# Performance work log

Hardware: AMD Instinct MI355X
Metric: run time of the kernel (lower is better)

The kernel has to match this reference:

```python
import jax, jax.numpy as jnp
import numpy as np

NUM_USERS = 1_000_000
NUM_ITEMS = 100_000
NUM_GROUPS = 500_000
EMB = 32           # forced by reshape (1, 4*32)
GROUP_SIZE = 3     # forced: 3 members + 1 item = 4 rows
B = 131_072


def setup_inputs() -> dict:
    key = jax.random.key(0)
    ks = jax.random.split(key, 12)
    return {
        "group_inputs": jax.random.randint(ks[0], (B,), 0, NUM_GROUPS),
        "item_inputs": jax.random.randint(ks[1], (B,), 0, NUM_ITEMS),
        "members": jax.random.randint(ks[2], (NUM_GROUPS, GROUP_SIZE), 0, NUM_USERS),
        "user_emb": jax.random.normal(ks[3], (NUM_USERS, EMB), jnp.float32) * 0.05,
        "item_emb": jax.random.normal(ks[4], (NUM_ITEMS, EMB - 18), jnp.float32) * 0.05,
        "genres": jax.random.uniform(ks[5], (NUM_ITEMS, 18), jnp.float32),
        "attn_W": jax.random.normal(ks[6], (4 * EMB, 3), jnp.float32) * 0.05,
        "attn_b": jax.random.normal(ks[7], (3,), jnp.float32) * 0.05,
        "pred_W1": jax.random.normal(ks[8], (3 * EMB, 8), jnp.float32) * 0.05,
        "pred_b1": jax.random.normal(ks[9], (8,), jnp.float32) * 0.05,
        "pred_W2": jax.random.normal(ks[10], (8, 1), jnp.float32) * 0.05,
        "pred_b2": jax.random.normal(ks[11], (1,), jnp.float32) * 0.05,
    }


def reference(group_inputs, item_inputs, members, user_emb, item_emb, genres,
              attn_W, attn_b, pred_W1, pred_b1, pred_W2, pred_b2):
    # item embedding: 14-d latent concat 18-d genre features -> [B, 32]
    it_e = jnp.concatenate([item_emb[item_inputs], genres[item_inputs]], axis=1)
    # members of each group -> [B, 3, 32]
    mem_e = user_emb[members[group_inputs]]
    # concat 3 member rows + 1 item row, flatten to [B, 128]
    gi = jnp.concatenate([mem_e, it_e[:, None, :]], axis=1).reshape(-1, 4 * EMB)
    # NOTE: source ConcatAttentionLayer returns the raw linear output (softmax
    # is computed but discarded), so attention "weights" are raw logits. [B, 3]
    at_wt = gi @ attn_W + attn_b
    # weighted sum of member embeddings -> [B, 32]
    g = jnp.einsum("bk,bkd->bd", at_wt, mem_e)
    new = jnp.concatenate([g * it_e, g, it_e], axis=1)  # [B, 96]
    h = jax.nn.relu(new @ pred_W1 + pred_b1)
    y = jax.nn.sigmoid(h @ pred_W2 + pred_b2)  # [B, 1]
    return y
```

## Files before the change

### kernel.cpp

```cpp
#include <hip/hip_runtime.h>
#include <math.h>

#define EMB 32

__global__ __launch_bounds__(256, 4) void bahdanau_fused(
    const int* __restrict__ group_inputs,
    const int* __restrict__ item_inputs,
    const int* __restrict__ members,
    const float* __restrict__ user_emb,
    const float* __restrict__ item_emb,
    const float* __restrict__ genres,
    const float* __restrict__ attn_W,
    const float* __restrict__ attn_b,
    const float* __restrict__ pred_W1,
    const float* __restrict__ pred_b1,
    const float* __restrict__ pred_W2,
    const float* __restrict__ pred_b2,
    float* __restrict__ out)
{
    __shared__ float s_aWT[3 * 128];
    __shared__ float s_W1T[8 * 96];
    __shared__ float s_ab[3];
    __shared__ float s_b1[8];
    __shared__ float s_W2[8];
    __shared__ float s_b2[1];

    const int tid = threadIdx.x;
    const int t = tid & 3;
    const int grp = tid >> 2;
    const int ebase = blockIdx.x * 128 + grp * 2;
    const int dbase = t * 8;

    const int g0 = group_inputs[ebase], g1 = group_inputs[ebase + 1];
    const int i0 = item_inputs[ebase],  i1 = item_inputs[ebase + 1];

    int m0[3], m1[3];
#pragma unroll
    for (int j = 0; j < 3; ++j) {
        m0[j] = members[3 * g0 + j];
        m1[j] = members[3 * g1 + j];
    }

    float itv0[8], itv1[8];
#pragma unroll
    for (int i = 0; i < 4; ++i) {
        const int d = dbase + 2 * i;
        const float2* p0 = (d < 14)
            ? (const float2*)(item_emb + (size_t)i0 * 14 + d)
            : (const float2*)(genres   + (size_t)i0 * 18 + (d - 14));
        const float2* p1 = (d < 14)
            ? (const float2*)(item_emb + (size_t)i1 * 14 + d)
            : (const float2*)(genres   + (size_t)i1 * 18 + (d - 14));
        const float2 a = *p0, b = *p1;
        itv0[2 * i]     = a.x; itv0[2 * i + 1] = a.y;
        itv1[2 * i]     = b.x; itv1[2 * i + 1] = b.y;
    }

    float mem0[3][8], mem1[3][8];
#pragma unroll
    for (int j = 0; j < 3; ++j) {
        const float4* p0 = (const float4*)(user_emb + (size_t)m0[j] * EMB + dbase);
        const float4* p1 = (const float4*)(user_emb + (size_t)m1[j] * EMB + dbase);
        float4 a = p0[0], b = p0[1], c = p1[0], d = p1[1];
        mem0[j][0] = a.x; mem0[j][1] = a.y; mem0[j][2] = a.z; mem0[j][3] = a.w;
        mem0[j][4] = b.x; mem0[j][5] = b.y; mem0[j][6] = b.z; mem0[j][7] = b.w;
        mem1[j][0] = c.x; mem1[j][1] = c.y; mem1[j][2] = c.z; mem1[j][3] = c.w;
        mem1[j][4] = d.x; mem1[j][5] = d.y; mem1[j][6] = d.z; mem1[j][7] = d.w;
    }

    for (int i = tid; i < 3 * 128; i += 256) {
        int k = i >> 7, d = i & 127;
        s_aWT[i] = attn_W[d * 3 + k];
    }
    for (int i = tid; i < 8 * 96; i += 256) {
        int c = i / 96, r = i - c * 96;
        s_W1T[i] = pred_W1[r * 8 + c];
    }
    if (tid < 3) s_ab[tid] = attn_b[tid];
    else if (tid < 11) s_b1[tid - 3] = pred_b1[tid - 3];
    else if (tid < 19) s_W2[tid - 11] = pred_W2[tid - 11];
    else if (tid == 19) s_b2[0] = pred_b2[0];
    __syncthreads();

    float aw0[3], aw1[3];
#pragma unroll
    for (int k = 0; k < 3; ++k) {
        float a0 = 0.f, a1 = 0.f;
#pragma unroll
        for (int j = 0; j < 3; ++j) {
            const float4* wp = (const float4*)&s_aWT[k * 128 + j * 32 + dbase];
            float4 wl = wp[0], wh = wp[1];
            float w[8] = {wl.x, wl.y, wl.z, wl.w, wh.x, wh.y, wh.z, wh.w};
#pragma unroll
            for (int i = 0; i < 8; ++i) {
                a0 = fmaf(mem0[j][i], w[i], a0);
                a1 = fmaf(mem1[j][i], w[i], a1);
            }
        }
        {
            const float4* wp = (const float4*)&s_aWT[k * 128 + 96 + dbase];
            float4 wl = wp[0], wh = wp[1];
            float w[8] = {wl.x, wl.y, wl.z, wl.w, wh.x, wh.y, wh.z, wh.w};
#pragma unroll
            for (int i = 0; i < 8; ++i) {
                a0 = fmaf(itv0[i], w[i], a0);
                a1 = fmaf(itv1[i], w[i], a1);
            }
        }
        aw0[k] = a0; aw1[k] = a1;
    }
#pragma unroll
    for (int k = 0; k < 3; ++k) {
        float v0 = aw0[k];
        v0 += __shfl_xor(v0, 1, 4);
        v0 += __shfl_xor(v0, 2, 4);
        aw0[k] = v0 + s_ab[k];
        float v1 = aw1[k];
        v1 += __shfl_xor(v1, 1, 4);
        v1 += __shfl_xor(v1, 2, 4);
        aw1[k] = v1 + s_ab[k];
    }

    float gv0[8], gv1[8], git0[8], git1[8];
#pragma unroll
    for (int i = 0; i < 8; ++i) {
        gv0[i] = aw0[0] * mem0[0][i] + aw0[1] * mem0[1][i] + aw0[2] * mem0[2][i];
        gv1[i] = aw1[0] * mem1[0][i] + aw1[1] * mem1[1][i] + aw1[2] * mem1[2][i];
        git0[i] = gv0[i] * itv0[i];
        git1[i] = gv1[i] * itv1[i];
    }

    float ph0[8], ph1[8];
#pragma unroll
    for (int c = 0; c < 8; ++c) {
        float a0 = 0.f, a1 = 0.f;
        const float4* wp0 = (const float4*)&s_W1T[c * 96 + dbase];
        const float4* wp1 = (const float4*)&s_W1T[c * 96 + 32 + dbase];
        const float4* wp2 = (const float4*)&s_W1T[c * 96 + 64 + dbase];
        float4 al = wp0[0], ah = wp0[1];
        float4 bl = wp1[0], bh = wp1[1];
        float4 cl = wp2[0], ch = wp2[1];
        float wa[8] = {al.x, al.y, al.z, al.w, ah.x, ah.y, ah.z, ah.w};
        float wb[8] = {bl.x, bl.y, bl.z, bl.w, bh.x, bh.y, bh.z, bh.w};
        float wc[8] = {cl.x, cl.y, cl.z, cl.w, ch.x, ch.y, ch.z, ch.w};
#pragma unroll
        for (int i = 0; i < 8; ++i) {
            a0 = fmaf(git0[i], wa[i], a0);
            a0 = fmaf(gv0[i],  wb[i], a0);
            a0 = fmaf(itv0[i], wc[i], a0);
            a1 = fmaf(git1[i], wa[i], a1);
            a1 = fmaf(gv1[i],  wb[i], a1);
            a1 = fmaf(itv1[i], wc[i], a1);
        }
        ph0[c] = a0; ph1[c] = a1;
    }

    float hq[8];
#pragma unroll
    for (int c = 0; c < 8; ++c) {
        float v0 = ph0[c];
        v0 += __shfl_xor(v0, 1, 4);
        v0 += __shfl_xor(v0, 2, 4);
        float v1 = ph1[c];
        v1 += __shfl_xor(v1, 1, 4);
        v1 += __shfl_xor(v1, 2, 4);
        hq[c] = (t == 0) ? v0 : v1;
    }

    if (t < 2) {
        float y = s_b2[0];
#pragma unroll
        for (int c = 0; c < 8; ++c) {
            float h = fmaxf(hq[c] + s_b1[c], 0.0f);
            y = fmaf(h, s_W2[c], y);
        }
        y = 1.0f / (1.0f + expf(-y));
        out[ebase + t] = y;
    }
}

extern "C" void kernel_launch(void* const* d_in, const int* in_sizes, int n_in,
                              void* d_out, int out_size, void* d_ws, size_t ws_size,
                              hipStream_t stream) {
    const int*   group_inputs = (const int*)d_in[0];
    const int*   item_inputs  = (const int*)d_in[1];
    const int*   members      = (const int*)d_in[2];
    const float* user_emb     = (const float*)d_in[3];
    const float* item_emb     = (const float*)d_in[4];
    const float* genres       = (const float*)d_in[5];
    const float* attn_W       = (const float*)d_in[6];
    const float* attn_b       = (const float*)d_in[7];
    const float* pred_W1      = (const float*)d_in[8];
    const float* pred_b1      = (const float*)d_in[9];
    const float* pred_W2      = (const float*)d_in[10];
    const float* pred_b2      = (const float*)d_in[11];
    float* out = (float*)d_out;

    const int B = in_sizes[0];
    const int blocks = B / 128;

    bahdanau_fused<<<blocks, 256, 0, stream>>>(
        group_inputs, item_inputs, members, user_emb, item_emb, genres,
        attn_W, attn_b, pred_W1, pred_b1, pred_W2, pred_b2, out);
}
```

Measured before the change: 208.6 us.

## Give each wavefront a private weight copy to drop block barrier and split element pipelines

```diff
diff --git a/kernel.cpp b/kernel.cpp
--- a/kernel.cpp
+++ b/kernel.cpp
@@ -18,22 +18,40 @@
     const float* __restrict__ pred_b2,
     float* __restrict__ out)
 {
-    __shared__ float s_aWT[3 * 128];
-    __shared__ float s_W1T[8 * 96];
-    __shared__ float s_ab[3];
-    __shared__ float s_b1[8];
-    __shared__ float s_W2[8];
-    __shared__ float s_b2[1];
-
-    const int tid = threadIdx.x;
+    __shared__ float smem[4 * 1184];
+
+    const int tid  = threadIdx.x;
+    const int lane = tid & 63;
+    float* sw = smem + (tid >> 6) * 1184;
+
     const int t = tid & 3;
     const int grp = tid >> 2;
     const int ebase = blockIdx.x * 128 + grp * 2;
     const int dbase = t * 8;
 
-    const int g0 = group_inputs[ebase], g1 = group_inputs[ebase + 1];
-    const int i0 = item_inputs[ebase],  i1 = item_inputs[ebase + 1];
-
+    const int2 gpair = *(const int2*)&group_inputs[ebase];
+    const int2 ipair = *(const int2*)&item_inputs[ebase];
+
+#pragma unroll
+    for (int it = 0; it < 19; ++it) {
+        const int i = lane + it * 64;
+        float v;
+        if (i < 384) {
+            const int k = i >> 7, d = i & 127;
+            v = attn_W[d * 3 + k];
+        } else if (i < 1152) {
+            const int r2 = i - 384, c = r2 / 96, r = r2 - c * 96;
+            v = pred_W1[r * 8 + c];
+        } else if (i < 1155) v = attn_b[i - 1152];
+        else if (i < 1163)   v = pred_b1[i - 1155];
+        else if (i < 1171)   v = pred_W2[i - 1163];
+        else                 v = pred_b2[0];
+        if (i < 1172) sw[i] = v;
+        else if (i < 1184) sw[i] = 0.0f;
+    }
+
+    const int g0 = gpair.x, g1 = gpair.y;
+    const int i0 = ipair.x, i1 = ipair.y;
     int m0[3], m1[3];
 #pragma unroll
     for (int j = 0; j < 3; ++j) {
@@ -48,132 +66,154 @@
         const float2* p0 = (d < 14)
             ? (const float2*)(item_emb + (size_t)i0 * 14 + d)
             : (const float2*)(genres   + (size_t)i0 * 18 + (d - 14));
+        const float2 a = *p0;
+        itv0[2 * i] = a.x; itv0[2 * i + 1] = a.y;
+    }
+#pragma unroll
+    for (int i = 0; i < 4; ++i) {
+        const int d = dbase + 2 * i;
         const float2* p1 = (d < 14)
             ? (const float2*)(item_emb + (size_t)i1 * 14 + d)
             : (const float2*)(genres   + (size_t)i1 * 18 + (d - 14));
-        const float2 a = *p0, b = *p1;
-        itv0[2 * i]     = a.x; itv0[2 * i + 1] = a.y;
-        itv1[2 * i]     = b.x; itv1[2 * i + 1] = b.y;
+        const float2 b = *p1;
+        itv1[2 * i] = b.x; itv1[2 * i + 1] = b.y;
     }
 
     float mem0[3][8], mem1[3][8];
 #pragma unroll
     for (int j = 0; j < 3; ++j) {
         const float4* p0 = (const float4*)(user_emb + (size_t)m0[j] * EMB + dbase);
-        const float4* p1 = (const float4*)(user_emb + (size_t)m1[j] * EMB + dbase);
-        float4 a = p0[0], b = p0[1], c = p1[0], d = p1[1];
+        float4 a = p0[0], b = p0[1];
         mem0[j][0] = a.x; mem0[j][1] = a.y; mem0[j][2] = a.z; mem0[j][3] = a.w;
         mem0[j][4] = b.x; mem0[j][5] = b.y; mem0[j][6] = b.z; mem0[j][7] = b.w;
+    }
+#pragma unroll
+    for (int j = 0; j < 3; ++j) {
+        const float4* p1 = (const float4*)(user_emb + (size_t)m1[j] * EMB + dbase);
+        float4 c = p1[0], d = p1[1];
         mem1[j][0] = c.x; mem1[j][1] = c.y; mem1[j][2] = c.z; mem1[j][3] = c.w;
         mem1[j][4] = d.x; mem1[j][5] = d.y; mem1[j][6] = d.z; mem1[j][7] = d.w;
     }
 
-    for (int i = tid; i < 3 * 128; i += 256) {
-        int k = i >> 7, d = i & 127;
-        s_aWT[i] = attn_W[d * 3 + k];
-    }
-    for (int i = tid; i < 8 * 96; i += 256) {
-        int c = i / 96, r = i - c * 96;
-        s_W1T[i] = pred_W1[r * 8 + c];
-    }
-    if (tid < 3) s_ab[tid] = attn_b[tid];
-    else if (tid < 11) s_b1[tid - 3] = pred_b1[tid - 3];
-    else if (tid < 19) s_W2[tid - 11] = pred_W2[tid - 11];
-    else if (tid == 19) s_b2[0] = pred_b2[0];
-    __syncthreads();
-
-    float aw0[3], aw1[3];
-#pragma unroll
-    for (int k = 0; k < 3; ++k) {
-        float a0 = 0.f, a1 = 0.f;
-#pragma unroll
-        for (int j = 0; j < 3; ++j) {
-            const float4* wp = (const float4*)&s_aWT[k * 128 + j * 32 + dbase];
+    float hq0, hq1;
+    {
+        float aw[3];
+#pragma unroll
+        for (int k = 0; k < 3; ++k) {
+            float a0 = 0.f;
+#pragma unroll
+            for (int j = 0; j < 3; ++j) {
+                const float4* wp = (const float4*)&sw[k * 128 + j * 32 + dbase];
+                float4 wl = wp[0], wh = wp[1];
+                float w[8] = {wl.x, wl.y, wl.z, wl.w, wh.x, wh.y, wh.z, wh.w};
+#pragma unroll
+                for (int i = 0; i < 8; ++i) a0 = fmaf(mem0[j][i], w[i], a0);
+            }
+            const float4* wp = (const float4*)&sw[k * 128 + 96 + dbase];
             float4 wl = wp[0], wh = wp[1];
             float w[8] = {wl.x, wl.y, wl.z, wl.w, wh.x, wh.y, wh.z, wh.w};
 #pragma unroll
+            for (int i = 0; i < 8; ++i) a0 = fmaf(itv0[i], w[i], a0);
+            a0 += __shfl_xor(a0, 1, 4);
+            a0 += __shfl_xor(a0, 2, 4);
+            aw[k] = a0 + sw[1152 + k];
+        }
+        float gv[8];
+#pragma unroll
+        for (int i = 0; i < 8; ++i)
+            gv[i] = aw[0] * mem0[0][i] + aw[1] * mem0[1][i] + aw[2] * mem0[2][i];
+        float ph[8];
+#pragma unroll
+        for (int c = 0; c < 8; ++c) {
+            const float4* wpa = (const float4*)&sw[384 + c * 96 + dbase];
+            const float4* wpb = (const float4*)&sw[384 + c * 96 + 32 + dbase];
+            const float4* wpc = (const float4*)&sw[384 + c * 96 + 64 + dbase];
+            float4 al = wpa[0], ah = wpa[1];
+            float4 bl = wpb[0], bh = wpb[1];
+            float4 cl = wpc[0], ch = wpc[1];
+            float wa[8] = {al.x, al.y, al.z, al.w, ah.x, ah.y, ah.z, ah.w};
+            float wb[8] = {bl.x, bl.y, bl.z, bl.w, bh.x, bh.y, bh.z, bh.w};
+            float wc[8] = {cl.x, cl.y, cl.z, cl.w, ch.x, ch.y, ch.z, ch.w};
+            float a0 = 0.f;
+#pragma unroll
             for (int i = 0; i < 8; ++i) {
-                a0 = fmaf(mem0[j][i], w[i], a0);
-                a1 = fmaf(mem1[j][i], w[i], a1);
-            }
-        }
-        {
-            const float4* wp = (const float4*)&s_aWT[k * 128 + 96 + dbase];
+                a0 = fmaf(gv[i], fmaf(itv0[i], wa[i], wb[i]), a0);
+                a0 = fmaf(itv0[i], wc[i], a0);
+            }
+            ph[c] = a0;
+        }
+        float y = sw[1171];
+#pragma unroll
+        for (int c = 0; c < 8; ++c) {
+            float v = ph[c];
+            v += __shfl_xor(v, 1, 4);
+            v += __shfl_xor(v, 2, 4);
+            float h = fmaxf(v + sw[1155 + c], 0.0f);
+            y = fmaf(h, sw[1163 + c], y);
+        }
+        hq0 = y;
+    }
+
+    {
+        float aw[3];
+#pragma unroll
+        for (int k = 0; k < 3; ++k) {
+            float a1 = 0.f;
+#pragma unroll
+            for (int j = 0; j < 3; ++j) {
+                const float4* wp = (const float4*)&sw[k * 128 + j * 32 + dbase];
+                float4 wl = wp[0], wh = wp[1];
+                float w[8] = {wl.x, wl.y, wl.z, wl.w, wh.x, wh.y, wh.z, wh.w};
+#pragma unroll
+                for (int i = 0; i < 8; ++i) a1 = fmaf(mem1[j][i], w[i], a1);
+            }
+            const float4* wp = (const float4*)&sw[k * 128 + 96 + dbase];
             float4 wl = wp[0], wh = wp[1];
             float w[8] = {wl.x, wl.y, wl.z, wl.w, wh.x, wh.y, wh.z, wh.w};
 #pragma unroll
+            for (int i = 0; i < 8; ++i) a1 = fmaf(itv1[i], w[i], a1);
+            a1 += __shfl_xor(a1, 1, 4);
+            a1 += __shfl_xor(a1, 2, 4);
+            aw[k] = a1 + sw[1152 + k];
+        }
+        float gv[8];
+#pragma unroll
+        for (int i = 0; i < 8; ++i)
+            gv[i] = aw[0] * mem1[0][i] + aw[1] * mem1[1][i] + aw[2] * mem1[2][i];
+        float ph[8];
+#pragma unroll
+        for (int c = 0; c < 8; ++c) {
+            const float4* wpa = (const float4*)&sw[384 + c * 96 + dbase];
+            const float4* wpb = (const float4*)&sw[384 + c * 96 + 32 + dbase];
+            const float4* wpc = (const float4*)&sw[384 + c * 96 + 64 + dbase];
+            float4 al = wpa[0], ah = wpa[1];
+            float4 bl = wpb[0], bh = wpb[1];
+            float4 cl = wpc[0], ch = wpc[1];
+            float wa[8] = {al.x, al.y, al.z, al.w, ah.x, ah.y, ah.z, ah.w};
+            float wb[8] = {bl.x, bl.y, bl.z, bl.w, bh.x, bh.y, bh.z, bh.w};
+            float wc[8] = {cl.x, cl.y, cl.z, cl.w, ch.x, ch.y, ch.z, ch.w};
+            float a1 = 0.f;
+#pragma unroll
             for (int i = 0; i < 8; ++i) {
-                a0 = fmaf(itv0[i], w[i], a0);
-                a1 = fmaf(itv1[i], w[i], a1);
-            }
-        }
-        aw0[k] = a0; aw1[k] = a1;
-    }
-#pragma unroll
-    for (int k = 0; k < 3; ++k) {
-        float v0 = aw0[k];
-        v0 += __shfl_xor(v0, 1, 4);
-        v0 += __shfl_xor(v0, 2, 4);
-        aw0[k] = v0 + s_ab[k];
-        float v1 = aw1[k];
-        v1 += __shfl_xor(v1, 1, 4);
-        v1 += __shfl_xor(v1, 2, 4);
-        aw1[k] = v1 + s_ab[k];
-    }
-
-    float gv0[8], gv1[8], git0[8], git1[8];
-#pragma unroll
-    for (int i = 0; i < 8; ++i) {
-        gv0[i] = aw0[0] * mem0[0][i] + aw0[1] * mem0[1][i] + aw0[2] * mem0[2][i];
-        gv1[i] = aw1[0] * mem1[0][i] + aw1[1] * mem1[1][i] + aw1[2] * mem1[2][i];
-        git0[i] = gv0[i] * itv0[i];
-        git1[i] = gv1[i] * itv1[i];
-    }
-
-    float ph0[8], ph1[8];
-#pragma unroll
-    for (int c = 0; c < 8; ++c) {
-        float a0 = 0.f, a1 = 0.f;
-        const float4* wp0 = (const float4*)&s_W1T[c * 96 + dbase];
-        const float4* wp1 = (const float4*)&s_W1T[c * 96 + 32 + dbase];
-        const float4* wp2 = (const float4*)&s_W1T[c * 96 + 64 + dbase];
-        float4 al = wp0[0], ah = wp0[1];
-        float4 bl = wp1[0], bh = wp1[1];
-        float4 cl = wp2[0], ch = wp2[1];
-        float wa[8] = {al.x, al.y, al.z, al.w, ah.x, ah.y, ah.z, ah.w};
-        float wb[8] = {bl.x, bl.y, bl.z, bl.w, bh.x, bh.y, bh.z, bh.w};
-        float wc[8] = {cl.x, cl.y, cl.z, cl.w, ch.x, ch.y, ch.z, ch.w};
-#pragma unroll
-        for (int i = 0; i < 8; ++i) {
-            a0 = fmaf(git0[i], wa[i], a0);
-            a0 = fmaf(gv0[i],  wb[i], a0);
-            a0 = fmaf(itv0[i], wc[i], a0);
-            a1 = fmaf(git1[i], wa[i], a1);
-            a1 = fmaf(gv1[i],  wb[i], a1);
-            a1 = fmaf(itv1[i], wc[i], a1);
-        }
-        ph0[c] = a0; ph1[c] = a1;
-    }
-
-    float hq[8];
-#pragma unroll
-    for (int c = 0; c < 8; ++c) {
-        float v0 = ph0[c];
-        v0 += __shfl_xor(v0, 1, 4);
-        v0 += __shfl_xor(v0, 2, 4);
-        float v1 = ph1[c];
-        v1 += __shfl_xor(v1, 1, 4);
-        v1 += __shfl_xor(v1, 2, 4);
-        hq[c] = (t == 0) ? v0 : v1;
+                a1 = fmaf(gv[i], fmaf(itv1[i], wa[i], wb[i]), a1);
+                a1 = fmaf(itv1[i], wc[i], a1);
+            }
+            ph[c] = a1;
+        }
+        float y = sw[1171];
+#pragma unroll
+        for (int c = 0; c < 8; ++c) {
+            float v = ph[c];
+            v += __shfl_xor(v, 1, 4);
+            v += __shfl_xor(v, 2, 4);
+            float h = fmaxf(v + sw[1155 + c], 0.0f);
+            y = fmaf(h, sw[1163 + c], y);
+        }
+        hq1 = y;
     }
 
     if (t < 2) {
-        float y = s_b2[0];
-#pragma unroll
-        for (int c = 0; c < 8; ++c) {
-            float h = fmaxf(hq[c] + s_b1[c], 0.0f);
-            y = fmaf(h, s_W2[c], y);
-        }
+        float y = (t == 0) ? hq0 : hq1;
         y = 1.0f / (1.0f + expf(-y));
         out[ebase + t] = y;
     }
```

New measurement: 216.6 us. +3.8%, slower.
